# Performance work log

Measured on AMD Instinct MI355X. Metric: run time of the kernel, lower is better.

Reference implementation:

```python
import jax, jax.numpy as jnp
import numpy as np

B, N, C, H, HD = 32, 512, 384, 6, 64
WH = WW = WT = 8
ALPHA = 4.0
KS = 5


def safe_pow(x, p):
    # x = relu(...) >= 0; avoid nan grads at x == 0
    pos = x > 0
    return jnp.where(pos, jnp.where(pos, x, 1.0) ** p, 0.0)


def setup_inputs() -> dict:
    key = jax.random.key(0)
    ks = jax.random.split(key, 12)
    s = 0.02
    return {
        "x": jax.random.normal(ks[0], (B, N, C), jnp.float32),
        "y": jax.random.normal(ks[1], (B, N, C), jnp.float32),
        "Wqkvg": jax.random.normal(ks[2], (4 * C, C), jnp.float32) * s,
        "bqkvg": jax.random.normal(ks[3], (4 * C,), jnp.float32) * s,
        "Wproj": jax.random.normal(ks[4], (C, C), jnp.float32) * s,
        "bproj": jax.random.normal(ks[5], (C,), jnp.float32) * s,
        "dwc_w": jax.random.normal(ks[6], (HD, 1, KS, KS, KS), jnp.float32) * s,
        "dwc_b": jax.random.normal(ks[7], (HD,), jnp.float32) * s,
        "power_p": jax.random.normal(ks[8], (1, H, 1, HD), jnp.float32) * s,
        "scale_p": jax.random.normal(ks[9], (1, 1, C), jnp.float32) * s,
        "pe": jax.random.normal(ks[10], (1, N, C), jnp.float32) * s,
    }


def reference(x, y, Wqkvg, bqkvg, Wproj, bproj, dwc_w, dwc_b, power_p, scale_p, pe):
    qkv = (x @ Wqkvg.T + bqkvg).reshape(B, N, 4, C)
    k = qkv[:, :, 1]
    v = qkv[:, :, 2]
    g = qkv[:, :, 3]
    q = (y @ Wqkvg.T + bqkvg).reshape(B, N, 4, C)[:, :, 0]

    k = k + pe
    scale = jax.nn.softplus(scale_p)          # (1,1,C)
    power = 1.0 + ALPHA * jax.nn.sigmoid(power_p)  # (1,H,1,HD)
    q = q / scale
    k = k / scale

    def heads(t):  # (B,N,C) -> (B,H,N,HD)
        return t.reshape(B, N, H, HD).transpose(0, 2, 1, 3)

    q = heads(q)
    k = heads(k)
    v = heads(v)

    q_pos = safe_pow(jax.nn.relu(q), power)
    q_neg = safe_pow(jax.nn.relu(-q), power)
    k_pos = safe_pow(jax.nn.relu(k), power)
    k_neg = safe_pow(jax.nn.relu(-k), power)

    q_sim = jnp.concatenate([q_pos, q_neg], axis=-1)   # (B,H,N,2HD)
    q_opp = jnp.concatenate([q_neg, q_pos], axis=-1)
    kf = jnp.concatenate([k_pos, k_neg], axis=-1)      # (B,H,N,2HD)
    v1, v2 = jnp.split(v, 2, axis=-1)                  # each (B,H,N,HD/2)

    k_mean = kf.mean(axis=-2)                          # (B,H,2HD)
    inv_sqrt_n = N ** (-0.5)
    kfs = kf * inv_sqrt_n

    z_sim = 1.0 / (jnp.einsum("bhnd,bhd->bhn", q_sim, k_mean)[..., None] + 1e-6)
    kv1 = jnp.einsum("bhnd,bhne->bhde", kfs, v1 * inv_sqrt_n)
    x_sim = jnp.einsum("bhnd,bhde->bhne", q_sim, kv1) * z_sim

    z_opp = 1.0 / (jnp.einsum("bhnd,bhd->bhn", q_opp, k_mean)[..., None] + 1e-6)
    kv2 = jnp.einsum("bhnd,bhne->bhde", kfs, v2 * inv_sqrt_n)
    x_opp = jnp.einsum("bhnd,bhde->bhne", q_opp, kv2) * z_opp

    xa = jnp.concatenate([x_sim, x_opp], axis=-1)      # (B,H,N,HD)
    xa = xa.transpose(0, 2, 1, 3).reshape(B, N, C)

    # depthwise conv3d on v: (B*H, HD, Wh, Ww, Wt)
    vr = v.reshape(B * H, WH, WW, WT, HD).transpose(0, 4, 1, 2, 3)
    pad = KS // 2
    vc = jax.lax.conv_general_dilated(
        vr, dwc_w, window_strides=(1, 1, 1),
        padding=[(pad, pad)] * 3,
        dimension_numbers=("NCDHW", "OIDHW", "NCDHW"),
        feature_group_count=HD,
    ) + dwc_b[None, :, None, None, None]
    vc = vc.transpose(0, 2, 3, 4, 1).reshape(B, N, C)

    out = (xa + vc) * g
    out = out @ Wproj.T + bproj
    return out
```

## Files before the change

### kernel.cpp

```cpp
#include <hip/hip_runtime.h>
#include <hip/hip_bf16.h>
#include <math.h>

#define B_  32
#define N_  512
#define C_  384
#define H_  6
#define HD_ 64
#define M_  (B_*N_)

typedef __attribute__((ext_vector_type(8))) short bfrag;
typedef __attribute__((ext_vector_type(8))) unsigned short u16x8;
typedef __attribute__((ext_vector_type(4))) float f32x4;

__device__ __forceinline__ unsigned short f2bfu(float f){
  unsigned int u = __float_as_uint(f);
  u += 0x7fffu + ((u >> 16) & 1u);
  return (unsigned short)(u >> 16);
}
__device__ __forceinline__ float bf2f(unsigned short u){
  return __uint_as_float(((unsigned int)u) << 16);
}
__device__ __forceinline__ bfrag cvt8(float4 a, float4 b){
  bfrag r;
  r[0]=(short)f2bfu(a.x); r[1]=(short)f2bfu(a.y); r[2]=(short)f2bfu(a.z); r[3]=(short)f2bfu(a.w);
  r[4]=(short)f2bfu(b.x); r[5]=(short)f2bfu(b.y); r[6]=(short)f2bfu(b.z); r[7]=(short)f2bfu(b.w);
  return r;
}
__device__ __forceinline__ void gload_lds16(const unsigned short* gp, unsigned short* lp){
  __builtin_amdgcn_global_load_lds(
      (const __attribute__((address_space(1))) void*)gp,
      (__attribute__((address_space(3))) void*)lp, 16, 0, 0);
}

__global__ void param_kernel(const float* __restrict__ scale_p,
                             const float* __restrict__ power_p,
                             float* __restrict__ scale_inv,
                             float* __restrict__ power){
  int t = threadIdx.x;
  if (t < C_){
    float s  = scale_p[t];
    scale_inv[t] = 1.0f / log1pf(expf(s));
  }
  if (t < H_*HD_){
    float p = power_p[t];
    power[t] = 1.0f + 4.0f / (1.0f + expf(-p));
  }
}

__global__ void sentinel_kernel(float* __restrict__ out, int n){
  int i = blockIdx.x*256 + threadIdx.x;
  if (i < n) out[i] = 1.0e9f;
}

__global__ __launch_bounds__(256) void cvt_bf16_kernel(
    const float* __restrict__ x, const float* __restrict__ y,
    const float* __restrict__ W, const float* __restrict__ Wp,
    unsigned short* __restrict__ xb, unsigned short* __restrict__ yb,
    unsigned short* __restrict__ Wb, unsigned short* __restrict__ Wpb)
{
  const int bid = blockIdx.x;
  const float* src; unsigned short* dst; int base;
  if (bid < 3072)      { src = x;  dst = xb;  base = bid; }
  else if (bid < 6144) { src = y;  dst = yb;  base = bid - 3072; }
  else if (bid < 6432) { src = W;  dst = Wb;  base = bid - 6144; }
  else                 { src = Wp; dst = Wpb; base = bid - 6432; }
  const size_t i0 = ((size_t)base*256 + threadIdx.x)*8;
  float4 a = *reinterpret_cast<const float4*>(src + i0);
  float4 b = *reinterpret_cast<const float4*>(src + i0 + 4);
  *reinterpret_cast<bfrag*>(dst + i0) = cvt8(a, b);
}

__global__ __launch_bounds__(256,4) void gemm_qkvg(
    const unsigned short* __restrict__ xb, const unsigned short* __restrict__ yb,
    const unsigned short* __restrict__ Wb, const float* __restrict__ bias,
    const float* __restrict__ pe, const float* __restrict__ scale_inv,
    const float* __restrict__ power,
    unsigned short* __restrict__ qf, unsigned short* __restrict__ kf,
    unsigned short* __restrict__ v, unsigned short* __restrict__ g)
{
  __shared__ __align__(16) unsigned short smem[16384];

  const int tid  = threadIdx.x;
  const int row0 = blockIdx.y * 128;
  const int col0 = blockIdx.x * 128;
  const int mode = blockIdx.x / 3;
  const unsigned short* Ab = (mode == 0) ? yb : xb;

  const int wave = tid >> 6, lane = tid & 63;
  const int wm = (wave >> 1) * 64, wn = (wave & 1) * 64;
  const int fr = lane & 15, quad = lane >> 4;
  const int srr = tid >> 2;
  const int skc = (tid & 3) * 8;

  const unsigned short* ga0 = &Ab[(size_t)(row0 + srr)*C_ + skc];
  const unsigned short* gb0 = &Wb[(size_t)(col0 + srr)*C_ + skc];
  const size_t gstep = (size_t)64*C_;

  f32x4 acc[4][4] = {};

  gload_lds16(ga0,         &smem[tid*8]);
  gload_lds16(ga0 + gstep, &smem[2048 + tid*8]);
  gload_lds16(gb0,         &smem[8192 + tid*8]);
  gload_lds16(gb0 + gstep, &smem[8192 + 2048 + tid*8]);
  __syncthreads();

  #pragma unroll 2
  for (int t = 0; t < 12; t++){
    const int cur = t & 1;
    if (t < 11){
      const int k0 = (t+1)*32;
      const int nxt = cur^1;
      gload_lds16(ga0 + k0,         &smem[nxt*4096 + tid*8]);
      gload_lds16(ga0 + gstep + k0, &smem[nxt*4096 + 2048 + tid*8]);
      gload_lds16(gb0 + k0,         &smem[8192 + nxt*4096 + tid*8]);
      gload_lds16(gb0 + gstep + k0, &smem[8192 + nxt*4096 + 2048 + tid*8]);
    }
    bfrag af[4], bf[4];
    #pragma unroll
    for (int f = 0; f < 4; f++){
      af[f] = *reinterpret_cast<const bfrag*>(&smem[cur*4096 + (wm + f*16 + fr)*32 + quad*8]);
      bf[f] = *reinterpret_cast<const bfrag*>(&smem[8192 + cur*4096 + (wn + f*16 + fr)*32 + quad*8]);
    }
    #pragma unroll
    for (int i=0;i<4;i++)
      #pragma unroll
      for (int j=0;j<4;j++)
        acc[i][j] = __builtin_amdgcn_mfma_f32_16x16x32_bf16(af[i], bf[j], acc[i][j], 0, 0, 0);
    __syncthreads();
  }

  const int cbase = col0 - mode*384;
  if (mode <= 1){
    unsigned short* dst = (mode == 0) ? qf : kf;
    #pragma unroll
    for (int i = 0; i < 4; i++){
      const int rowb = row0 + wm + i*16 + quad*4;
      #pragma unroll
      for (int j = 0; j < 4; j++){
        const int cl = wn + j*16 + fr;
        const int cc = cbase + cl;
        const int hh = cc >> 6, dd = cc & 63;
        const float bcol = bias[mode*384 + cc];
        const float scv  = scale_inv[cc];
        const float p    = power[cc];
        #pragma unroll
        for (int r = 0; r < 4; r++){
          const int row = rowb + r;
          float val = acc[i][j][r] + bcol;
          if (mode == 1) val += pe[(row & (N_-1))*C_ + cc];
          val *= scv;
          const float ax = fabsf(val);
          const float pv = (ax > 0.0f) ? exp2f(p * log2f(ax)) : 0.0f;
          const unsigned int pos = f2bfu((val > 0.0f) ? pv : 0.0f);
          const unsigned int neg = f2bfu((val < 0.0f) ? pv : 0.0f);
          *reinterpret_cast<unsigned int*>(&dst[(size_t)row*768 + hh*128 + dd*2]) =
              pos | (neg << 16);
        }
      }
    }
  } else {
    unsigned short* dst = (mode == 2) ? v : g;
    #pragma unroll
    for (int i = 0; i < 4; i++){
      const int rowb = row0 + wm + i*16 + quad*4;
      #pragma unroll
      for (int j = 0; j < 4; j++){
        const int cc = cbase + wn + j*16 + fr;
        const float bcol = bias[mode*384 + cc];
        #pragma unroll
        for (int r = 0; r < 4; r++)
          dst[(size_t)(rowb + r)*C_ + cc] = f2bfu(acc[i][j][r] + bcol);
      }
    }
  }
}

#define NC_ 256
__global__ __launch_bounds__(512) void attn_kernel(
    const unsigned short* __restrict__ qf, const unsigned short* __restrict__ kf,
    const unsigned short* __restrict__ v, float* __restrict__ xa)
{
  const int bh = blockIdx.x;
  const int b = bh / H_, h = bh % H_;
  __shared__ __align__(16) unsigned short smem[54912];
  unsigned short* kfT  = smem;
  unsigned short* vT   = smem + 33792;
  unsigned short* kvBT = smem;
  unsigned short* qs   = smem + 33792;

  const int tid = threadIdx.x;
  const int wave = tid >> 6, lane = tid & 63;
  const int fr = lane & 15, quad = lane >> 4;

  const unsigned short* kfg   = kf + (size_t)b*N_*768 + h*128;
  const unsigned short* vbase = v  + (size_t)b*N_*C_  + h*HD_;

  for (int i = tid; i < 16*NC_; i += 512){
    int e = 64 + (i >> 8);
    int nl = i & (NC_-1);
    vT[e*264 + nl] = (e == 64) ? (unsigned short)0x3F80 : (unsigned short)0;
  }
  __syncthreads();

  f32x4 acc[5] = {};
  for (int chunk = 0; chunk < 2; chunk++){
    const int n0 = chunk * NC_;
    for (int it = 0; it < 8; it++){
      int flat = it*512 + tid;
      int cg = flat & 15, nl = flat >> 4;
      int swz = cg << 3;
      u16x8 k8 = *reinterpret_cast<const u16x8*>(&kfg[(size_t)(n0+nl)*768 + cg*8]);
      #pragma unroll
      for (int j = 0; j < 8; j++) kfT[(cg*8+j)*264 + (nl ^ swz)] = k8[j];
    }
    for (int it = 0; it < 4; it++){
      int flat = it*512 + tid;
      int cg = flat & 7, nl = flat >> 3;
      int swz = cg << 3;
      u16x8 v8 = *reinterpret_cast<const u16x8*>(&vbase[(size_t)(n0+nl)*C_ + cg*8]);
      #pragma unroll
      for (int j = 0; j < 8; j++) vT[(cg*8+j)*264 + (nl ^ swz)] = v8[j];
    }
    __syncthreads();
    const int arow = wave*16 + fr;
    const int aswz = (arow >> 3) << 3;
    for (int kk = 0; kk < NC_/32; kk++){
      int ko = kk*32 + quad*8;
      bfrag af = *reinterpret_cast<const bfrag*>(&kfT[arow*264 + (ko ^ aswz)]);
      #pragma unroll
      for (int j = 0; j < 5; j++){
        const int brow = j*16 + fr;
        const int bswz = (brow >> 3) << 3;
        bfrag bfr = *reinterpret_cast<const bfrag*>(&vT[brow*264 + (ko ^ bswz)]);
        acc[j] = __builtin_amdgcn_mfma_f32_16x16x32_bf16(af, bfr, acc[j], 0, 0, 0);
      }
    }
    __syncthreads();
  }

  const float invN = 1.0f / (float)N_;
  {
    const int dbase = wave*16 + quad*4;
    #pragma unroll
    for (int j = 0; j < 4; j++){
      const int e = j*16 + fr;
      const unsigned short c0 = f2bfu(acc[j][0] * invN);
      const unsigned short c1 = f2bfu(acc[j][1] * invN);
      const unsigned short c2 = f2bfu(acc[j][2] * invN);
      const unsigned short c3 = f2bfu(acc[j][3] * invN);
      ushort4 w4;
      if (e < 32){ w4.x=c0; w4.y=c1; w4.z=c2; w4.w=c3; }
      else       { w4.x=c1; w4.y=c0; w4.z=c3; w4.w=c2; }
      *reinterpret_cast<ushort4*>(&kvBT[e*136 + dbase]) = w4;
    }
    if (fr == 0){
      const unsigned short k0 = f2bfu(acc[4][0] * invN);
      const unsigned short k1 = f2bfu(acc[4][1] * invN);
      const unsigned short k2 = f2bfu(acc[4][2] * invN);
      const unsigned short k3 = f2bfu(acc[4][3] * invN);
      ushort4 wk;  wk.x=k0;  wk.y=k1;  wk.z=k2;  wk.w=k3;
      ushort4 wkf; wkf.x=k1; wkf.y=k0; wkf.z=k3; wkf.w=k2;
      *reinterpret_cast<ushort4*>(&kvBT[64*136 + dbase]) = wk;
      *reinterpret_cast<ushort4*>(&kvBT[65*136 + dbase]) = wkf;
    }
  }
  __syncthreads();

  const unsigned short* qfg = qf + (size_t)b*N_*768 + h*128;
  float* xabase = xa + (size_t)b*N_*C_ + h*HD_;
  for (int mc = 0; mc < 4; mc++){
    const int m0 = mc * 128;
    for (int it = 0; it < 4; it++){
      int flat = it*512 + tid;
      int cg = flat & 15, nl = flat >> 4;
      *reinterpret_cast<u16x8*>(&qs[nl*136 + cg*8]) =
          *reinterpret_cast<const u16x8*>(&qfg[(size_t)(m0+nl)*768 + cg*8]);
    }
    __syncthreads();
    f32x4 a2[5] = {};
    for (int kk = 0; kk < 4; kk++){
      int ko = kk*32 + quad*8;
      bfrag af = *reinterpret_cast<const bfrag*>(&qs[(wave*16 + fr)*136 + ko]);
      #pragma unroll
      for (int j = 0; j < 5; j++){
        bfrag bfr = *reinterpret_cast<const bfrag*>(&kvBT[(j*16 + fr)*136 + ko]);
        a2[j] = __builtin_amdgcn_mfma_f32_16x16x32_bf16(af, bfr, a2[j], 0, 0, 0);
      }
    }
    #pragma unroll
    for (int r = 0; r < 4; r++){
      const float zsim = __shfl(a2[4][r], quad*16);
      const float zopp = __shfl(a2[4][r], quad*16 + 1);
      const int n = m0 + wave*16 + quad*4 + r;
      #pragma unroll
      for (int j = 0; j < 4; j++){
        const int e = j*16 + fr;
        const float z = (e < 32) ? zsim : zopp;
        xabase[(size_t)n*C_ + e] = a2[j][r] / (z + 1e-6f);
      }
    }
    __syncthreads();
  }
}

__global__ __launch_bounds__(512) void conv_kernel(
    const unsigned short* __restrict__ v, const float* __restrict__ dwc_w,
    const float* __restrict__ dwc_b, const float* __restrict__ xa,
    const unsigned short* __restrict__ g, unsigned short* __restrict__ ab)
{
  const int bh = blockIdx.x;
  const int b = bh / H_, h = bh % H_;
  const int ch0 = blockIdx.y * 16;
  __shared__ float vol[16][521];
  __shared__ float wv[16][126];
  __shared__ float wb[16];
  const int tid = threadIdx.x;
  const unsigned short* vbase = v + (size_t)b*N_*C_ + h*HD_;
  const float* xabatch = xa + (size_t)b*N_*C_ + (size_t)h*N_*HD_;
  const unsigned short* gb = g + (size_t)b*N_*C_ + (size_t)h*N_*HD_;
  unsigned short* abb = ab + (size_t)b*N_*C_ + (size_t)h*N_*HD_;

  for (int it = 0; it < 16; it++){
    int flat = it*512 + tid;
    int cl = flat & 15, n = flat >> 4;
    vol[cl][n] = bf2f(vbase[(size_t)n*C_ + ch0 + cl]);
  }
  for (int i = tid; i < 16*125; i += 512){
    int ch = i / 125, wi = i - ch*125;
    wv[ch][wi] = dwc_w[(ch0+ch)*125 + wi];
  }
  if (tid < 16) wb[tid] = dwc_b[ch0 + tid];
  __syncthreads();

  for (int t = 0; t < 2; t++){
    const int task = t*512 + tid;
    const int ch = task & 15;
    const int zy = task >> 4;
    const int z = zy >> 3, yc = zy & 7;
    float o[8];
    const float bias = wb[ch];
    #pragma unroll
    for (int xx = 0; xx < 8; xx++) o[xx] = bias;
    #pragma unroll
    for (int kd = 0; kd < 5; kd++){
      const int zz = z + kd - 2;
      if ((unsigned)zz >= 8u) continue;
      #pragma unroll
      for (int kh = 0; kh < 5; kh++){
        const int yy = yc + kh - 2;
        if ((unsigned)yy >= 8u) continue;
        const float* row = &vol[ch][zz*64 + yy*8];
        float rr[8];
        #pragma unroll
        for (int xx = 0; xx < 8; xx++) rr[xx] = row[xx];
        const float* wrow = &wv[ch][kd*25 + kh*5];
        float w5[5];
        #pragma unroll
        for (int kw = 0; kw < 5; kw++) w5[kw] = wrow[kw];
        #pragma unroll
        for (int xx = 0; xx < 8; xx++){
          #pragma unroll
          for (int kw = 0; kw < 5; kw++){
            const int xi = xx + kw - 2;
            if ((unsigned)xi < 8u) o[xx] = fmaf(w5[kw], rr[xi], o[xx]);
          }
        }
      }
    }
    const int nb = zy * 8;
    #pragma unroll
    for (int xx = 0; xx < 8; xx++){
      const size_t di = (size_t)(nb + xx)*HD_ + ch0 + ch;
      abb[di] = f2bfu((xabatch[di] + o[xx]) * bf2f(gb[di]));
    }
  }
}

__global__ __launch_bounds__(256,4) void proj_kernel(
    const unsigned short* __restrict__ ab, const unsigned short* __restrict__ Wpb,
    const float* __restrict__ bp, float* __restrict__ out)
{
  __shared__ unsigned short As[2][4096];
  __shared__ unsigned short Bs[2][4096];

  const int tid  = threadIdx.x;
  const int row0 = blockIdx.y * 128;
  const int col0 = blockIdx.x * 128;
  const int wave = tid >> 6, lane = tid & 63;
  const int wm = (wave >> 1) * 64, wn = (wave & 1) * 64;
  const int fr = lane & 15, quad = lane >> 4;
  const int srr = tid >> 2;
  const int skc = (tid & 3) * 8;

  const unsigned short* ga0 = &ab[(size_t)(row0 + srr)*C_ + skc];
  const unsigned short* gb0 = &Wpb[(size_t)(col0 + srr)*C_ + skc];
  const size_t gstep = (size_t)64*C_;

  f32x4 acc[4][4] = {};

  gload_lds16(ga0,         &As[0][tid*8]);
  gload_lds16(ga0 + gstep, &As[0][2048 + tid*8]);
  gload_lds16(gb0,         &Bs[0][tid*8]);
  gload_lds16(gb0 + gstep, &Bs[0][2048 + tid*8]);
  __syncthreads();

  #pragma unroll 2
  for (int t = 0; t < 12; t++){
    const int cur = t & 1;
    if (t < 11){
      const int k0 = (t+1)*32;
      gload_lds16(ga0 + k0,         &As[cur^1][tid*8]);
      gload_lds16(ga0 + gstep + k0, &As[cur^1][2048 + tid*8]);
      gload_lds16(gb0 + k0,         &Bs[cur^1][tid*8]);
      gload_lds16(gb0 + gstep + k0, &Bs[cur^1][2048 + tid*8]);
    }
    bfrag af[4], bf[4];
    #pragma unroll
    for (int f = 0; f < 4; f++){
      af[f] = *reinterpret_cast<const bfrag*>(&As[cur][(wm + f*16 + fr)*32 + quad*8]);
      bf[f] = *reinterpret_cast<const bfrag*>(&Bs[cur][(wn + f*16 + fr)*32 + quad*8]);
    }
    #pragma unroll
    for (int i=0;i<4;i++)
      #pragma unroll
      for (int j=0;j<4;j++)
        acc[i][j] = __builtin_amdgcn_mfma_f32_16x16x32_bf16(af[i], bf[j], acc[i][j], 0, 0, 0);
    __syncthreads();
  }

  #pragma unroll
  for (int i = 0; i < 4; i++){
    const int rowb = row0 + wm + i*16 + quad*4;
    #pragma unroll
    for (int j = 0; j < 4; j++){
      const int col = col0 + wn + j*16 + fr;
      const float bcol = bp[col];
      #pragma unroll
      for (int r = 0; r < 4; r++)
        out[(size_t)(rowb + r)*C_ + col] = acc[i][j][r] + bcol;
    }
  }
}

extern "C" void kernel_launch(void* const* d_in, const int* in_sizes, int n_in,
                              void* d_out, int out_size, void* d_ws, size_t ws_size,
                              hipStream_t stream){
  float* out = (float*)d_out;

  const int expect[11] = {6291456, 6291456, 589824, 1536, 147456, 384, 8000, 64, 384, 384, 196608};
  bool ok = (n_in == 11);
  for (int i = 0; ok && i < 11; i++) ok = (in_sizes[i] == expect[i]);
  if (!ok){
    sentinel_kernel<<<(out_size+255)/256, 256, 0, stream>>>(out, out_size);
    return;
  }

  const float* x    = (const float*)d_in[0];
  const float* y    = (const float*)d_in[1];
  const float* W    = (const float*)d_in[2];
  const float* bq   = (const float*)d_in[3];
  const float* Wp   = (const float*)d_in[4];
  const float* bp   = (const float*)d_in[5];
  const float* dwcw = (const float*)d_in[6];
  const float* dwcb = (const float*)d_in[7];
  const float* pwp  = (const float*)d_in[8];
  const float* scp  = (const float*)d_in[9];
  const float* pe   = (const float*)d_in[10];

  float* ws = (float*)d_ws;
  const size_t SZ = (size_t)M_ * C_;
  unsigned short* qf  = (unsigned short*)ws;
  unsigned short* kfb = qf + 2*SZ;
  unsigned short* v   = (unsigned short*)(ws + 2*SZ);
  unsigned short* g   = v + SZ;
  unsigned short* xb  = (unsigned short*)(ws + 3*SZ);
  unsigned short* yb  = xb + SZ;
  float* xa = ws + 3*SZ;
  unsigned short* ab  = (unsigned short*)ws;
  unsigned short* Wb  = (unsigned short*)(ws + 4*SZ);
  unsigned short* Wpb = Wb + 589824;
  float* scale_inv = (float*)(Wpb + 147456);
  float* power     = scale_inv + 512;

  param_kernel<<<1, 512, 0, stream>>>(scp, pwp, scale_inv, power);
  cvt_bf16_kernel<<<6504, 256, 0, stream>>>(x, y, W, Wp, xb, yb, Wb, Wpb);
  gemm_qkvg<<<dim3(12, 128), 256, 0, stream>>>(xb, yb, Wb, bq, pe, scale_inv, power, qf, kfb, v, g);
  attn_kernel<<<dim3(B_*H_), 512, 0, stream>>>(qf, kfb, v, xa);
  conv_kernel<<<dim3(B_*H_, 4), 512, 0, stream>>>(v, dwcw, dwcb, xa, g, ab);
  proj_kernel<<<dim3(3, 128), 256, 0, stream>>>(ab, Wpb, bp, out);
}
```

Before: 239.8 us.

## Remap GEMM block order, register-prefetch attention loads, swizzle kv LDS, vectorize conv loads

```diff
diff --git a/kernel.cpp b/kernel.cpp
--- a/kernel.cpp
+++ b/kernel.cpp
@@ -82,9 +82,13 @@
   __shared__ __align__(16) unsigned short smem[16384];
 
   const int tid  = threadIdx.x;
-  const int row0 = blockIdx.y * 128;
-  const int col0 = blockIdx.x * 128;
-  const int mode = blockIdx.x / 3;
+  const int bid0 = blockIdx.y * 12 + blockIdx.x;
+  const int nb   = (bid0 & 7) * 192 + (bid0 >> 3);
+  const int by   = nb / 12;
+  const int bx   = nb - by * 12;
+  const int row0 = by * 128;
+  const int col0 = bx * 128;
+  const int mode = bx / 3;
   const unsigned short* Ab = (mode == 0) ? yb : xb;
 
   const int wave = tid >> 6, lane = tid & 63;
@@ -187,7 +191,6 @@
   unsigned short* kfT  = smem;
   unsigned short* vT   = smem + 33792;
   unsigned short* kvBT = smem;
-  unsigned short* qs   = smem + 33792;
 
   const int tid = threadIdx.x;
   const int wave = tid >> 6, lane = tid & 63;
@@ -201,28 +204,22 @@
     int nl = i & (NC_-1);
     vT[e*264 + nl] = (e == 64) ? (unsigned short)0x3F80 : (unsigned short)0;
   }
-  __syncthreads();
-
-  f32x4 acc[5] = {};
-  for (int chunk = 0; chunk < 2; chunk++){
-    const int n0 = chunk * NC_;
+
+  auto storeA = [&](bfrag* kr, bfrag* vr){
+    #pragma unroll
     for (int it = 0; it < 8; it++){
-      int flat = it*512 + tid;
-      int cg = flat & 15, nl = flat >> 4;
-      int swz = cg << 3;
-      u16x8 k8 = *reinterpret_cast<const u16x8*>(&kfg[(size_t)(n0+nl)*768 + cg*8]);
-      #pragma unroll
-      for (int j = 0; j < 8; j++) kfT[(cg*8+j)*264 + (nl ^ swz)] = k8[j];
-    }
+      int flat = it*512 + tid; int cg = flat & 15, nl = flat >> 4; int swz = cg << 3;
+      #pragma unroll
+      for (int j = 0; j < 8; j++) kfT[(cg*8+j)*264 + (nl ^ swz)] = (unsigned short)kr[it][j];
+    }
+    #pragma unroll
     for (int it = 0; it < 4; it++){
-      int flat = it*512 + tid;
-      int cg = flat & 7, nl = flat >> 3;
-      int swz = cg << 3;
-      u16x8 v8 = *reinterpret_cast<const u16x8*>(&vbase[(size_t)(n0+nl)*C_ + cg*8]);
-      #pragma unroll
-      for (int j = 0; j < 8; j++) vT[(cg*8+j)*264 + (nl ^ swz)] = v8[j];
-    }
-    __syncthreads();
+      int flat = it*512 + tid; int cg = flat & 7, nl = flat >> 3; int swz = cg << 3;
+      #pragma unroll
+      for (int j = 0; j < 8; j++) vT[(cg*8+j)*264 + (nl ^ swz)] = (unsigned short)vr[it][j];
+    }
+  };
+  auto mfmaA = [&](f32x4* acc){
     const int arow = wave*16 + fr;
     const int aswz = (arow >> 3) << 3;
     for (int kk = 0; kk < NC_/32; kk++){
@@ -236,8 +233,31 @@
         acc[j] = __builtin_amdgcn_mfma_f32_16x16x32_bf16(af, bfr, acc[j], 0, 0, 0);
       }
     }
-    __syncthreads();
-  }
+  };
+
+  bfrag kr0[8], vr0[4], kr1[8], vr1[4];
+  #pragma unroll
+  for (int it = 0; it < 8; it++){ int flat = it*512 + tid; int cg = flat & 15, nl = flat >> 4;
+    kr0[it] = *reinterpret_cast<const bfrag*>(&kfg[(size_t)nl*768 + cg*8]); }
+  #pragma unroll
+  for (int it = 0; it < 4; it++){ int flat = it*512 + tid; int cg = flat & 7, nl = flat >> 3;
+    vr0[it] = *reinterpret_cast<const bfrag*>(&vbase[(size_t)nl*C_ + cg*8]); }
+  storeA(kr0, vr0);
+  #pragma unroll
+  for (int it = 0; it < 8; it++){ int flat = it*512 + tid; int cg = flat & 15, nl = flat >> 4;
+    kr1[it] = *reinterpret_cast<const bfrag*>(&kfg[(size_t)(NC_+nl)*768 + cg*8]); }
+  #pragma unroll
+  for (int it = 0; it < 4; it++){ int flat = it*512 + tid; int cg = flat & 7, nl = flat >> 3;
+    vr1[it] = *reinterpret_cast<const bfrag*>(&vbase[(size_t)(NC_+nl)*C_ + cg*8]); }
+
+  __syncthreads();
+  f32x4 acc[5] = {};
+  mfmaA(acc);
+  __syncthreads();
+  storeA(kr1, vr1);
+  __syncthreads();
+  mfmaA(acc);
+  __syncthreads();
 
   const float invN = 1.0f / (float)N_;
   {
@@ -252,7 +272,8 @@
       ushort4 w4;
       if (e < 32){ w4.x=c0; w4.y=c1; w4.z=c2; w4.w=c3; }
       else       { w4.x=c1; w4.y=c0; w4.z=c3; w4.w=c2; }
-      *reinterpret_cast<ushort4*>(&kvBT[e*136 + dbase]) = w4;
+      const int col = dbase ^ (((e >> 3) & 7) << 3);
+      *reinterpret_cast<ushort4*>(&kvBT[e*136 + col]) = w4;
     }
     if (fr == 0){
       const unsigned short k0 = f2bfu(acc[4][0] * invN);
@@ -269,25 +290,35 @@
 
   const unsigned short* qfg = qf + (size_t)b*N_*768 + h*128;
   float* xabase = xa + (size_t)b*N_*C_ + h*HD_;
+  const int qrow = wave*16 + fr;
+  bfrag qv0[4], qv1[4];
+  #pragma unroll
+  for (int kk = 0; kk < 4; kk++)
+    qv0[kk] = *reinterpret_cast<const bfrag*>(&qfg[(size_t)qrow*768 + kk*32 + quad*8]);
+
+  #pragma unroll
   for (int mc = 0; mc < 4; mc++){
-    const int m0 = mc * 128;
-    for (int it = 0; it < 4; it++){
-      int flat = it*512 + tid;
-      int cg = flat & 15, nl = flat >> 4;
-      *reinterpret_cast<u16x8*>(&qs[nl*136 + cg*8]) =
-          *reinterpret_cast<const u16x8*>(&qfg[(size_t)(m0+nl)*768 + cg*8]);
-    }
-    __syncthreads();
+    bfrag* qcur = (mc & 1) ? qv1 : qv0;
+    bfrag* qnxt = (mc & 1) ? qv0 : qv1;
+    if (mc < 3){
+      const int m1 = (mc+1) * 128;
+      #pragma unroll
+      for (int kk = 0; kk < 4; kk++)
+        qnxt[kk] = *reinterpret_cast<const bfrag*>(&qfg[(size_t)(m1+qrow)*768 + kk*32 + quad*8]);
+    }
     f32x4 a2[5] = {};
+    #pragma unroll
     for (int kk = 0; kk < 4; kk++){
       int ko = kk*32 + quad*8;
-      bfrag af = *reinterpret_cast<const bfrag*>(&qs[(wave*16 + fr)*136 + ko]);
       #pragma unroll
       for (int j = 0; j < 5; j++){
-        bfrag bfr = *reinterpret_cast<const bfrag*>(&kvBT[(j*16 + fr)*136 + ko]);
-        a2[j] = __builtin_amdgcn_mfma_f32_16x16x32_bf16(af, bfr, a2[j], 0, 0, 0);
+        const int brow = j*16 + fr;
+        const int bsz = ((brow >> 3) & 7) << 3;
+        bfrag bfr = *reinterpret_cast<const bfrag*>(&kvBT[brow*136 + (ko ^ bsz)]);
+        a2[j] = __builtin_amdgcn_mfma_f32_16x16x32_bf16(qcur[kk], bfr, a2[j], 0, 0, 0);
       }
     }
+    const int m0 = mc * 128;
     #pragma unroll
     for (int r = 0; r < 4; r++){
       const float zsim = __shfl(a2[4][r], quad*16);
@@ -300,7 +331,6 @@
         xabase[(size_t)n*C_ + e] = a2[j][r] / (z + 1e-6f);
       }
     }
-    __syncthreads();
   }
 }
 
@@ -321,10 +351,13 @@
   const unsigned short* gb = g + (size_t)b*N_*C_ + (size_t)h*N_*HD_;
   unsigned short* abb = ab + (size_t)b*N_*C_ + (size_t)h*N_*HD_;
 
-  for (int it = 0; it < 16; it++){
+  #pragma unroll
+  for (int it = 0; it < 2; it++){
     int flat = it*512 + tid;
-    int cl = flat & 15, n = flat >> 4;
-    vol[cl][n] = bf2f(vbase[(size_t)n*C_ + ch0 + cl]);
+    int co = flat & 1, n = flat >> 1;
+    u16x8 v8 = *reinterpret_cast<const u16x8*>(&vbase[(size_t)n*C_ + ch0 + co*8]);
+    #pragma unroll
+    for (int j = 0; j < 8; j++) vol[co*8+j][n] = bf2f(v8[j]);
   }
   for (int i = tid; i < 16*125; i += 512){
     int ch = i / 125, wi = i - ch*125;
@@ -385,8 +418,12 @@
   __shared__ unsigned short Bs[2][4096];
 
   const int tid  = threadIdx.x;
-  const int row0 = blockIdx.y * 128;
-  const int col0 = blockIdx.x * 128;
+  const int bid0 = blockIdx.y * 3 + blockIdx.x;
+  const int nb   = (bid0 & 7) * 48 + (bid0 >> 3);
+  const int by   = nb / 3;
+  const int bx   = nb - by * 3;
+  const int row0 = by * 128;
+  const int col0 = bx * 128;
   const int wave = tid >> 6, lane = tid & 63;
   const int wm = (wave >> 1) * 64, wn = (wave & 1) * 64;
   const int fr = lane & 15, quad = lane >> 4;
```

Result: faster. 224.8 us, median of 2 (-6.2%).
